# Kernel optimization log

Measured on AMD Instinct MI355X. Metric: run time of the kernel, lower is better.

## Reference

```python
import jax, jax.numpy as jnp
import numpy as np

BETA = 0.25
COMMIT_W = 1.0


def setup_inputs() -> dict:
    key = jax.random.key(0)
    ks = jax.random.split(key, 6)
    B, N, DIM, CDIM, K = 8, 1024, 256, 64, 16384
    z = jax.random.normal(ks[0], (B, N, DIM), dtype=jnp.float32)
    Wq = jax.random.normal(ks[1], (CDIM, DIM), dtype=jnp.float32) * (DIM ** -0.5)
    bq = jax.random.normal(ks[2], (CDIM,), dtype=jnp.float32) * 0.01
    # torch init: uniform(-1/K, 1/K)
    emb = jax.random.uniform(ks[3], (K, CDIM), dtype=jnp.float32, minval=-1.0 / K, maxval=1.0 / K)
    Wp = jax.random.normal(ks[4], (DIM, CDIM), dtype=jnp.float32) * (CDIM ** -0.5)
    bp = jax.random.normal(ks[5], (DIM,), dtype=jnp.float32) * 0.01
    return {"z": z, "Wq": Wq, "bq": bq, "emb": emb, "Wp": Wp, "bp": bp}


def reference(z, Wq, bq, emb, Wp, bp):
    # quant projection: [B,N,dim] -> [B,N,cdim]
    zp = jnp.einsum('bnd,cd->bnc', z, Wq) + bq
    # squared euclidean distances to codebook: [B,N,K]
    d = (jnp.sum(zp * zp, axis=2, keepdims=True)
         + jnp.sum(emb * emb, axis=1)
         - 2.0 * jnp.einsum('bnc,kc->bnk', zp, emb))
    sample_idxs = jnp.argmin(d, axis=2)              # [B,N] int
    z_q = emb[sample_idxs]                            # [B,N,cdim]
    commit_loss = (jnp.mean((jax.lax.stop_gradient(z_q) - zp) ** 2)
                   + BETA * jnp.mean((z_q - jax.lax.stop_gradient(zp)) ** 2))
    commit_loss = COMMIT_W * commit_loss
    # straight-through estimator
    z_q = zp + jax.lax.stop_gradient(z_q - zp)
    # post-quant projection: [B,N,cdim] -> [B,N,dim]
    out = jnp.einsum('bnc,dc->bnd', z_q, Wp) + bp
    return out, sample_idxs, commit_loss
```

## Files before the change

### kernel.cpp

```cpp
#include <hip/hip_runtime.h>
#include <hip/hip_bf16.h>


#define VWIN 1.0e-5f
#define CMAX 16

typedef short short8v __attribute__((ext_vector_type(8)));
typedef float floatx16 __attribute__((ext_vector_type(16)));

__device__ __forceinline__ short f2bf(float x) {
    unsigned u = __builtin_bit_cast(unsigned, x);
    unsigned r = (u + 0x7fffu + ((u >> 16) & 1u)) >> 16;
    return (short)r;
}

__device__ __forceinline__ float np_pairwise64_sq(const float* __restrict__ p) {
    #pragma clang fp contract(off)
    float v[16];
#pragma unroll
    for (int j = 0; j < 16; ++j) {
        float x0 = p[j]      * p[j];
        float x1 = p[j + 32] * p[j + 32];
        float x2 = p[j + 16] * p[j + 16];
        float x3 = p[j + 48] * p[j + 48];
        float r0 = x0 + x1;
        float r1 = x2 + x3;
        v[j] = r0 + r1;
    }
    float s[8], t[4];
#pragma unroll
    for (int j = 0; j < 8; ++j) s[j] = v[j] + v[j + 8];
#pragma unroll
    for (int j = 0; j < 4; ++j) t[j] = s[j] + s[j + 4];
    return (t[0] + t[2]) + (t[1] + t[3]);
}

__global__ __launch_bounds__(512) void k_prep(const float* __restrict__ z,
                                              const float* __restrict__ Wq,
                                              const float* __restrict__ bq,
                                              const float* __restrict__ emb,
                                              float* __restrict__ zp32,
                                              float* __restrict__ A32,
                                              short8v* __restrict__ zpf,
                                              float* __restrict__ B32,
                                              short8v* __restrict__ ef,
                                              float* __restrict__ bfl,
                                              float4* __restrict__ embT4,
                                              int tokblocks, int K) {
    __shared__ float pool[64 * 129 + 32 * 128 + 32 * 65];
    const int tid = threadIdx.x;
    const int bx  = blockIdx.x;

    if (bx < tokblocks) {
        float* wq  = pool;
        float* zl  = pool + 64 * 129;
        float* zps = zl + 32 * 128;
        const int w    = tid >> 6;
        const int lane = tid & 63;
        const int tbase = bx * 32;

        float l[4][4];
#pragma unroll
        for (int i = 0; i < 4; ++i)
#pragma unroll
            for (int j = 0; j < 4; ++j) l[i][j] = 0.f;

        for (int h = 0; h < 2; ++h) {
            __syncthreads();
            for (int i = tid; i < 64 * 128; i += 512) {
                const int c = i >> 7, m = i & 127;
                wq[c * 129 + m] = Wq[(size_t)c * 256 + h * 128 + m];
            }
            for (int i = tid; i < 32 * 128; i += 512) {
                const int t = i >> 7, m = i & 127;
                zl[t * 128 + m] = z[(size_t)(tbase + t) * 256 + h * 128 + m];
            }
            __syncthreads();
            {
                #pragma clang fp contract(off)
                const float* wr  = wq + lane * 129;
                const float* zt0 = zl + (w * 4 + 0) * 128;
                const float* zt1 = zl + (w * 4 + 1) * 128;
                const float* zt2 = zl + (w * 4 + 2) * 128;
                const float* zt3 = zl + (w * 4 + 3) * 128;
                for (int m = 0; m < 128; m += 4) {
                    const float w0 = wr[m], w1 = wr[m + 1], w2 = wr[m + 2], w3 = wr[m + 3];
                    const float4 p0 = *(const float4*)(zt0 + m);
                    const float4 p1 = *(const float4*)(zt1 + m);
                    const float4 p2 = *(const float4*)(zt2 + m);
                    const float4 p3 = *(const float4*)(zt3 + m);
                    l[0][0] += p0.x * w0; l[0][1] += p0.y * w1; l[0][2] += p0.z * w2; l[0][3] += p0.w * w3;
                    l[1][0] += p1.x * w0; l[1][1] += p1.y * w1; l[1][2] += p1.z * w2; l[1][3] += p1.w * w3;
                    l[2][0] += p2.x * w0; l[2][1] += p2.y * w1; l[2][2] += p2.z * w2; l[2][3] += p2.w * w3;
                    l[3][0] += p3.x * w0; l[3][1] += p3.y * w1; l[3][2] += p3.z * w2; l[3][3] += p3.w * w3;
                }
            }
        }
        {
            #pragma clang fp contract(off)
            const float bqc = bq[lane];
#pragma unroll
            for (int tk = 0; tk < 4; ++tk) {
                const float acc = (l[tk][0] + l[tk][1]) + (l[tk][2] + l[tk][3]);
                const float zpv = acc + bqc;
                zp32[(size_t)(tbase + w * 4 + tk) * 64 + lane] = zpv;
                zps[(w * 4 + tk) * 65 + lane] = zpv;
            }
        }
        __syncthreads();
        if (tid < 32) A32[tbase + tid] = np_pairwise64_sq(zps + tid * 65);
        if (tid < 256) {
            const int fl = tid & 63;
            const int s  = tid >> 6;
            const int row = fl & 31;
            const int k0 = s * 16 + (fl >> 5) * 8;
            short8v hv;
            const float* p = zps + row * 65 + k0;
#pragma unroll
            for (int j = 0; j < 8; ++j) hv[j] = f2bf(p[j]);
            zpf[(size_t)(bx * 4 + s) * 64 + fl] = hv;
        }
    } else {
        const int half = tid >> 8;
        const int ltid = tid & 255;
        const int tile = (bx - tokblocks) * 2 + half;
        float* et = pool + half * (32 * 65);

        for (int i = ltid; i < 2048; i += 256)
            et[(i >> 6) * 65 + (i & 63)] = emb[(size_t)tile * 2048 + i];
        __syncthreads();
        if (ltid < 32) {
            const float b = np_pairwise64_sq(et + ltid * 65);
            B32[tile * 32 + ltid] = b;
            const unsigned hb = (unsigned)(unsigned short)f2bf(-0.5f * b);
            bfl[tile * 32 + ltid] = __builtin_bit_cast(float, hb << 16);
        }
        {
            const int fl = ltid & 63;
            const int s  = ltid >> 6;
            const int row = fl & 31;
            const int k0 = s * 16 + (fl >> 5) * 8;
            short8v hv;
            const float* p = et + row * 65 + k0;
#pragma unroll
            for (int j = 0; j < 8; ++j) hv[j] = f2bf(p[j]);
            ef[(size_t)(tile * 4 + s) * 64 + fl] = hv;
        }
#pragma unroll
        for (int p = 0; p < 2; ++p) {
            const int id = ltid + (p << 8);
            const int m4 = id >> 5;
            const int r  = id & 31;
            const float* q = et + r * 65 + m4 * 4;
            float4 v;
            v.x = q[0]; v.y = q[1]; v.z = q[2]; v.w = q[3];
            embT4[(size_t)m4 * K + tile * 32 + r] = v;
        }
    }
}

__global__ __launch_bounds__(256) void k_scan_max(const short8v* __restrict__ zpf,
                                                  const short8v* __restrict__ ef,
                                                  const float* __restrict__ bfl,
                                                  float* __restrict__ pmax32,
                                                  float* __restrict__ pslice_t,
                                                  int tokens, int K) {
    __shared__ short8v s_ef[2048];
    __shared__ float s_bfl[256];
    const int tid  = threadIdx.x;
    const int w    = tid >> 6;
    const int lane = tid & 63;
    const int half = lane >> 5;
    const int col  = lane & 31;
    const int ttb  = (blockIdx.x * 4 + w) * 4;
    const int etiles = K / 2048;
    const int ct0 = blockIdx.y * etiles;

    for (int i = tid; i < etiles * 256; i += 256) s_ef[i] = ef[(size_t)ct0 * 256 + i];
    for (int i = tid; i < etiles * 32;  i += 256) s_bfl[i] = bfl[ct0 * 32 + i];

    short8v zh[4][4];
#pragma unroll
    for (int q = 0; q < 4; ++q)
#pragma unroll
        for (int s = 0; s < 4; ++s) zh[q][s] = zpf[(size_t)((ttb + q) * 4 + s) * 64 + lane];

    __syncthreads();

    float macc[4] = {-3.0e38f, -3.0e38f, -3.0e38f, -3.0e38f};

    for (int it = 0; it < etiles; ++it) {
        short8v eh[4];
#pragma unroll
        for (int s = 0; s < 4; ++s) eh[s] = s_ef[it * 256 + s * 64 + lane];
        floatx16 binit;
#pragma unroll
        for (int r = 0; r < 16; ++r)
            binit[r] = s_bfl[it * 32 + (r & 3) + 8 * (r >> 2) + 4 * half];
#pragma unroll
        for (int q = 0; q < 4; ++q) {
            floatx16 acc = __builtin_amdgcn_mfma_f32_32x32x16_bf16(eh[0], zh[q][0], binit, 0, 0, 0);
#pragma unroll
            for (int s = 1; s < 4; ++s)
                acc = __builtin_amdgcn_mfma_f32_32x32x16_bf16(eh[s], zh[q][s], acc, 0, 0, 0);
            float t0 = fmaxf(acc[0], acc[1]),  t1 = fmaxf(acc[2], acc[3]);
            float t2 = fmaxf(acc[4], acc[5]),  t3 = fmaxf(acc[6], acc[7]);
            float t4 = fmaxf(acc[8], acc[9]),  t5 = fmaxf(acc[10], acc[11]);
            float t6 = fmaxf(acc[12], acc[13]), t7 = fmaxf(acc[14], acc[15]);
            t0 = fmaxf(t0, t1); t2 = fmaxf(t2, t3); t4 = fmaxf(t4, t5); t6 = fmaxf(t6, t7);
            float tm = fmaxf(fmaxf(t0, t2), fmaxf(t4, t6));
            tm = fmaxf(tm, __shfl_xor(tm, 32));
            macc[q] = fmaxf(macc[q], tm);
            if (half == 0) {
                const int tok = (ttb + q) * 32 + col;
                pmax32[(size_t)(ct0 + it) * tokens + tok] = tm;
            }
        }
    }

    if (half == 0) {
#pragma unroll
        for (int q = 0; q < 4; ++q) {
            const int tok = (ttb + q) * 32 + col;
            pslice_t[(size_t)tok * 64 + blockIdx.y] = macc[q];
        }
    }
}

__global__ __launch_bounds__(256) void k_refine_ct(const float4* __restrict__ embT4,
                                                   const float* __restrict__ emb,
                                                   const float* __restrict__ zp32,
                                                   const float* __restrict__ A32,
                                                   const float* __restrict__ B32,
                                                   const float* __restrict__ pslice_t,
                                                   const float* __restrict__ pmax32,
                                                   int tokens, int CT, int K,
                                                   int* __restrict__ idx,
                                                   float* __restrict__ out_idx,
                                                   double* __restrict__ ploss) {
    #pragma clang fp contract(off)
    __shared__ __align__(16) float zps[8 * 64];
    __shared__ int s_cand[8][CMAX];
    const int tid = threadIdx.x;
    const int tbase = blockIdx.x * 8;
    for (int i = tid; i < 512; i += 256) zps[i] = zp32[(size_t)tbase * 64 + i];
    __syncthreads();

    const int w   = tid >> 6;
    const int ln  = tid & 31;
    const int sub = (tid >> 5) & 1;
    const int g   = w * 2 + sub;
    const int t   = tbase + g;
    const int shift = sub * 32;

    const float sv0 = pslice_t[(size_t)t * 64 + ln];
    const float sv1 = pslice_t[(size_t)t * 64 + 32 + ln];
    float m = fmaxf(sv0, sv1);
#pragma unroll
    for (int off = 16; off; off >>= 1) m = fmaxf(m, __shfl_xor(m, off, 32));
    const float thv = m - VWIN;

    const unsigned q0 = (unsigned)(__ballot(sv0 >= thv) >> shift);
    const unsigned q1 = (unsigned)(__ballot(sv1 >= thv) >> shift);
    unsigned long long qs = (unsigned long long)q0 | ((unsigned long long)q1 << 32);

    int ncand = 0;
    while (qs) {
        const int s = __builtin_ctzll(qs);
        qs &= qs - 1;
        float pv = -3.0e38f;
        if (ln < 8) pv = pmax32[(size_t)(s * 8 + ln) * tokens + t];
        unsigned cm = (unsigned)(__ballot(pv >= thv) >> shift) & 0xffu;
        while (cm) {
            const int c = __builtin_ctz(cm);
            cm &= cm - 1;
            if (ncand < CMAX && ln == 0) s_cand[g][ncand] = s * 8 + c;
            ++ncand;
        }
    }

    const bool full = (ncand > CMAX);
    const int iters = full ? CT : ncand;

    const float A = A32[t];
    const float* zp = zps + g * 64;

    float best = 3.0e38f;
    int bj = 0x7fffffff;
    for (int i = 0; i < iters; ++i) {
        const int ct = full ? i : s_cand[g][i];
        const int j  = ct * 32 + ln;
        const float Bj = B32[j];
        float l0 = 0.f, l1 = 0.f, l2 = 0.f, l3 = 0.f;
#pragma unroll
        for (int m4 = 0; m4 < 16; ++m4) {
            const float4 ev = embT4[(size_t)m4 * K + j];
            const float4 zv = *(const float4*)(zp + m4 * 4);
            l0 += zv.x * ev.x;
            l1 += zv.y * ev.y;
            l2 += zv.z * ev.z;
            l3 += zv.w * ev.w;
        }
        const float M = (l0 + l1) + (l2 + l3);
        const float S = A + Bj;
        const float d = S - 2.f * M;
        if (d < best) { best = d; bj = j; }
    }

#pragma unroll
    for (int off = 16; off; off >>= 1) {
        const float od = __shfl_xor(best, off, 32);
        const int   oj = __shfl_xor(bj, off, 32);
        if (od < best || (od == best && oj < bj)) { best = od; bj = oj; }
    }
    if ((unsigned)bj >= (unsigned)K) bj = 0;

    const float e0 = emb[(size_t)bj * 64 + ln];
    const float e1 = emb[(size_t)bj * 64 + 32 + ln];
    const float df0 = e0 - zp[ln];
    const float df1 = e1 - zp[32 + ln];
    double ls = (double)df0 * (double)df0 + (double)df1 * (double)df1;
#pragma unroll
    for (int off = 16; off; off >>= 1) ls += __shfl_xor(ls, off, 32);

    if (ln == 0) {
        idx[t] = bj;
        out_idx[t] = (float)bj;
        ploss[t] = ls;
    }
}

__global__ __launch_bounds__(256) void k_out_v2(const float* __restrict__ emb,
                                                const float* __restrict__ zp32,
                                                const int* __restrict__ idx,
                                                const float* __restrict__ Wp,
                                                const float* __restrict__ bp,
                                                float* __restrict__ out,
                                                const double* __restrict__ ploss,
                                                float* __restrict__ out_loss,
                                                int tokens, int K,
                                                double denom, int do_loss) {
    __shared__ float zq[8 * 64];
    __shared__ double red[256];
    const int tid = threadIdx.x;
    const int tbase = blockIdx.x * 8;
    for (int i = tid; i < 512; i += 256) {
        const int tk = i >> 6, c = i & 63;
        const int t = tbase + tk;
        int k = idx[t];
        if ((unsigned)k >= (unsigned)K) k = 0;
        const float zpv = zp32[(size_t)t * 64 + c];
        zq[i] = zpv + (emb[(size_t)k * 64 + c] - zpv);
    }
    float4 wp[16];
#pragma unroll
    for (int i = 0; i < 16; ++i) wp[i] = *(const float4*)(Wp + (size_t)tid * 64 + i * 4);
    const float bpd = bp[tid];
    __syncthreads();
#pragma unroll
    for (int tk = 0; tk < 8; ++tk) {
        const float* zr = zq + tk * 64;
        float acc = 0.f;
#pragma unroll
        for (int i = 0; i < 16; ++i) {
            const float4 p = *(const float4*)(zr + i * 4);
            acc += p.x * wp[i].x + p.y * wp[i].y + p.z * wp[i].z + p.w * wp[i].w;
        }
        out[(size_t)(tbase + tk) * 256 + tid] = acc + bpd;
    }
    if (do_loss && blockIdx.x == 0) {
        double a = 0.0;
        for (int i = tid; i < tokens; i += 256) a += ploss[i];
        red[tid] = a;
        __syncthreads();
        for (int s = 128; s > 0; s >>= 1) {
            if (tid < s) red[tid] += red[tid + s];
            __syncthreads();
        }
        if (tid == 0) *out_loss = (float)(1.25 * red[0] / denom);
    }
}

__global__ __launch_bounds__(256) void k_loss_red(const double* __restrict__ ploss,
                                                  float* __restrict__ out_loss,
                                                  int tokens, double denom) {
    __shared__ double red[256];
    double a = 0.0;
    for (int i = threadIdx.x; i < tokens; i += 256) a += ploss[i];
    red[threadIdx.x] = a;
    __syncthreads();
    for (int s = 128; s > 0; s >>= 1) {
        if (threadIdx.x < s) red[threadIdx.x] += red[threadIdx.x + s];
        __syncthreads();
    }
    if (threadIdx.x == 0) *out_loss = (float)(1.25 * red[0] / denom);
}

__global__ __launch_bounds__(64) void k_zp_np(const float* __restrict__ z,
                                              const float* __restrict__ Wq,
                                              const float* __restrict__ bq,
                                              float* __restrict__ zp32,
                                              int DIN, int CD) {
    #pragma clang fp contract(off)
    extern __shared__ float zl[];
    const int t = blockIdx.x;
    const int tid = threadIdx.x;
    for (int i = tid; i < DIN; i += 64) zl[i] = z[(size_t)t * DIN + i];
    __syncthreads();
    const int main8 = DIN & ~7;
    for (int c = tid; c < CD; c += 64) {
        const float* wr = Wq + (size_t)c * DIN;
        float l0 = 0.f, l1 = 0.f, l2 = 0.f, l3 = 0.f;
        for (int m = 0; m < main8; m += 4) {
            l0 += zl[m]     * wr[m];
            l1 += zl[m + 1] * wr[m + 1];
            l2 += zl[m + 2] * wr[m + 2];
            l3 += zl[m + 3] * wr[m + 3];
        }
        float acc = (l0 + l1) + (l2 + l3);
        for (int i = main8; i < DIN; ++i) acc += zl[i] * wr[i];
        zp32[(size_t)t * CD + c] = acc + bq[c];
    }
}

__global__ __launch_bounds__(256) void k_rowsum2_np(const float* __restrict__ src,
                                                    float* __restrict__ dst,
                                                    int rows) {
    #pragma clang fp contract(off)
    const int r = blockIdx.x * 256 + threadIdx.x;
    if (r >= rows) return;
    dst[r] = np_pairwise64_sq(src + (size_t)r * 64);
}

__global__ __launch_bounds__(256) void k_rowsum2_gen(const float* __restrict__ src,
                                                     float* __restrict__ dst,
                                                     int rows, int CD) {
    #pragma clang fp contract(off)
    const int r = blockIdx.x * 256 + threadIdx.x;
    if (r >= rows) return;
    const float* p = src + (size_t)r * CD;
    if (CD < 8) {
        float a = 0.f;
        for (int i = 0; i < CD; ++i) a += p[i] * p[i];
        dst[r] = a;
        return;
    }
    float acc[8];
#pragma unroll
    for (int j = 0; j < 8; ++j) acc[j] = p[j] * p[j];
    const int main8 = CD & ~7;
    for (int i = 8; i < main8; i += 8)
#pragma unroll
        for (int j = 0; j < 8; ++j) acc[j] += p[i + j] * p[i + j];
    float res = ((acc[0] + acc[1]) + (acc[2] + acc[3])) + ((acc[4] + acc[5]) + (acc[6] + acc[7]));
    for (int i = main8; i < CD; ++i) res += p[i] * p[i];
    dst[r] = res;
}

__global__ __launch_bounds__(256) void k_scan_gen(const float* __restrict__ emb,
                                                  const float* __restrict__ zp32,
                                                  const float* __restrict__ A32,
                                                  const float* __restrict__ B32,
                                                  int* __restrict__ idx,
                                                  float* __restrict__ out_idx,
                                                  int K, int CD) {
    #pragma clang fp contract(off)
    extern __shared__ float sm[];
    float* zp = sm;
    float* rm = zp + CD;
    int*   rj = (int*)(rm + 256);
    const int t = blockIdx.x;
    const int tid = threadIdx.x;
    for (int i = tid; i < CD; i += 256) zp[i] = zp32[(size_t)t * CD + i];
    __syncthreads();
    const float A = A32[t];
    float m1 = 3.0e38f; int j1 = 0x7fffffff;
    const int main8 = CD & ~7;
    for (int k = tid; k < K; k += 256) {
        const float* e = emb + (size_t)k * CD;
        float l0 = 0.f, l1 = 0.f, l2 = 0.f, l3 = 0.f;
        for (int m = 0; m < main8; m += 4) {
            l0 += zp[m]     * e[m];
            l1 += zp[m + 1] * e[m + 1];
            l2 += zp[m + 2] * e[m + 2];
            l3 += zp[m + 3] * e[m + 3];
        }
        float M = (l0 + l1) + (l2 + l3);
        for (int i = main8; i < CD; ++i) M += zp[i] * e[i];
        float S = A + B32[k];
        float d = S - 2.f * M;
        if (d < m1) { m1 = d; j1 = k; }
    }
    rm[tid] = m1; rj[tid] = j1;
    __syncthreads();
    if (tid == 0) {
        float gm = 3.0e38f; int gj = 0x7fffffff;
        for (int s = 0; s < 256; ++s) {
            if (rm[s] < gm || (rm[s] == gm && rj[s] < gj)) { gm = rm[s]; gj = rj[s]; }
        }
        idx[t] = gj;
        out_idx[t] = (float)gj;
    }
}

__global__ __launch_bounds__(256) void k_out(const float* __restrict__ emb,
                                             const float* __restrict__ zp32,
                                             const int* __restrict__ idx,
                                             const float* __restrict__ Wp,
                                             const float* __restrict__ bp,
                                             float* __restrict__ out,
                                             int DOUT, int CD) {
    extern __shared__ float zq[];
    const int t = blockIdx.x;
    const int tid = threadIdx.x;
    const int k = idx[t];
    for (int i = tid; i < CD; i += 256) {
        const float zpv = zp32[(size_t)t * CD + i];
        zq[i] = zpv + (emb[(size_t)k * CD + i] - zpv);
    }
    __syncthreads();
    for (int d = tid; d < DOUT; d += 256) {
        const float* w = Wp + (size_t)d * CD;
        float acc = 0.f;
        for (int c = 0; c < CD; ++c) acc += zq[c] * w[c];
        out[(size_t)t * DOUT + d] = acc + bp[d];
    }
}

__global__ __launch_bounds__(256) void k_loss1(const float* __restrict__ zp32,
                                               const float* __restrict__ emb,
                                               const int* __restrict__ idx,
                                               double* __restrict__ part,
                                               long long total, int CD) {
    double acc = 0.0;
    const long long stride = (long long)gridDim.x * 256;
    for (long long e = (long long)blockIdx.x * 256 + threadIdx.x; e < total; e += stride) {
        const long long t = e / CD;
        const int c = (int)(e - t * CD);
        const float df = emb[(size_t)idx[t] * CD + c] - zp32[e];
        acc += (double)df * (double)df;
    }
    __shared__ double red[256];
    red[threadIdx.x] = acc;
    __syncthreads();
    for (int s = 128; s > 0; s >>= 1) {
        if (threadIdx.x < s) red[threadIdx.x] += red[threadIdx.x + s];
        __syncthreads();
    }
    if (threadIdx.x == 0) part[blockIdx.x] = red[0];
}

__global__ __launch_bounds__(256) void k_loss2(const double* __restrict__ part,
                                               float* __restrict__ out_loss,
                                               double denom, int n) {
    __shared__ double red[256];
    const int tid = threadIdx.x;
    red[tid] = (tid < n) ? part[tid] : 0.0;
    __syncthreads();
    for (int s = 128; s > 0; s >>= 1) {
        if (tid < s) red[tid] += red[tid + s];
        __syncthreads();
    }
    if (tid == 0) *out_loss = (float)(1.25 * red[0] / denom);
}

extern "C" void kernel_launch(void* const* d_in, const int* in_sizes, int n_in,
                              void* d_out, int out_size, void* d_ws, size_t ws_size,
                              hipStream_t stream) {
    const float* z   = (const float*)d_in[0];
    const float* Wq  = (const float*)d_in[1];
    const float* bq  = (const float*)d_in[2];
    const float* emb = (const float*)d_in[3];
    const float* Wp  = (const float*)d_in[4];
    const float* bp  = (const float*)d_in[5];

    const int CD   = in_sizes[2];
    const int DIN  = in_sizes[1] / CD;
    const int DOUT = in_sizes[5];
    const int K    = in_sizes[3] / CD;
    const long long T = (long long)in_sizes[0] / DIN;

    float* out      = (float*)d_out;
    float* out_idx  = out + (size_t)T * DOUT;
    float* out_loss = out_idx + T;

    char* ws = (char*)d_ws;
    size_t off = 0;
    auto carve = [&](size_t bytes) -> char* {
        char* p = ws + off;
        off = (off + bytes + 255) & ~(size_t)255;
        return p;
    };
    float*  zp32  = (float*)carve((size_t)T * CD * 4);
    float*  A32   = (float*)carve((size_t)T * 4);
    float*  B32   = (float*)carve((size_t)K * 4);
    int*    idx   = (int*)carve((size_t)T * 4);
    double* part  = (double*)carve(128 * 8);
    double* ploss = (double*)carve((size_t)T * 8);

    bool fast = (CD == 64) && (DIN == 256) && (K % 2048 == 0) && (K <= 16384) &&
                (T % 512 == 0);
    short8v* zpf = nullptr; short8v* ef = nullptr;
    float* bfl = nullptr; float* pmax32 = nullptr; float* pslice_t = nullptr;
    float4* embT4 = nullptr;
    const int NSLICE = 64;
    const int CT = K / 32;
    if (fast) {
        const int ztiles = (int)(T / 32);
        const int ctiles = CT;
        zpf      = (short8v*)carve((size_t)ztiles * 256 * 16);
        ef       = (short8v*)carve((size_t)ctiles * 256 * 16);
        bfl      = (float*)carve((size_t)ctiles * 32 * 4);
        pmax32   = (float*)carve((size_t)CT * T * 4);
        pslice_t = (float*)carve((size_t)T * NSLICE * 4);
        embT4    = (float4*)carve((size_t)K * 64 * 4);
        if (off > ws_size) fast = false;
    }

    if (fast) {
        const int tokblocks  = (int)(T / 32);
        const int codeblocks = K / 64;
        k_prep<<<dim3((unsigned)(tokblocks + codeblocks)), dim3(512), 0, stream>>>(
            z, Wq, bq, emb, zp32, A32, zpf, B32, ef, bfl, embT4, tokblocks, K);

        dim3 grid((unsigned)(T / 512), NSLICE);
        k_scan_max<<<grid, dim3(256), 0, stream>>>(zpf, ef, bfl, pmax32, pslice_t,
                                                   (int)T, K);

        k_refine_ct<<<dim3((unsigned)(T / 8)), dim3(256), 0, stream>>>(
            embT4, emb, zp32, A32, B32, pslice_t, pmax32, (int)T, CT, K,
            idx, out_idx, ploss);

        if (DOUT == 256 && T % 8 == 0) {
            k_out_v2<<<dim3((unsigned)(T / 8)), dim3(256), 0, stream>>>(
                emb, zp32, idx, Wp, bp, out, ploss, out_loss, (int)T, K,
                (double)T * CD, 1);
        } else {
            k_loss_red<<<dim3(1), dim3(256), 0, stream>>>(ploss, out_loss, (int)T,
                                                          (double)T * CD);
            k_out<<<dim3((unsigned)T), dim3(256), (size_t)CD * 4, stream>>>(
                emb, zp32, idx, Wp, bp, out, DOUT, CD);
        }
    } else {
        k_zp_np<<<dim3((unsigned)T), dim3(64), (size_t)DIN * 4, stream>>>(z, Wq, bq, zp32, DIN, CD);
        if (CD == 64)
            k_rowsum2_np<<<dim3((unsigned)((T + 255) / 256)), dim3(256), 0, stream>>>(zp32, A32, (int)T);
        else
            k_rowsum2_gen<<<dim3((unsigned)((T + 255) / 256)), dim3(256), 0, stream>>>(zp32, A32, (int)T, CD);
        if (CD == 64)
            k_rowsum2_np<<<dim3((K + 255) / 256), dim3(256), 0, stream>>>(emb, B32, K);
        else
            k_rowsum2_gen<<<dim3((K + 255) / 256), dim3(256), 0, stream>>>(emb, B32, K, CD);

        const size_t sm = (size_t)CD * 4 + 256 * 4 + 256 * 4;
        k_scan_gen<<<dim3((unsigned)T), dim3(256), sm, stream>>>(
            emb, zp32, A32, B32, idx, out_idx, K, CD);
        k_loss1<<<dim3(128), dim3(256), 0, stream>>>(zp32, emb, idx, part, (long long)T * CD, CD);
        k_loss2<<<dim3(1), dim3(256), 0, stream>>>(part, out_loss, (double)T * CD, 128);

        if (DOUT == 256 && CD == 64 && T % 8 == 0) {
            k_out_v2<<<dim3((unsigned)(T / 8)), dim3(256), 0, stream>>>(
                emb, zp32, idx, Wp, bp, out, ploss, out_loss, (int)T, K,
                (double)T * CD, 0);
        } else {
            k_out<<<dim3((unsigned)T), dim3(256), (size_t)CD * 4, stream>>>(
                emb, zp32, idx, Wp, bp, out, DOUT, CD);
        }
    }
}
```

Measured before the change: 145.6 us.

## Fuse refine and output projection into one tail kernel with atomic loss reduction

Merges the candidate-refine kernel and the output projection kernel into a single k_tail launch. Indices and zp stay in shared memory instead of round-tripping through global buffers. The commit loss is now reduced with double atomics plus a last-block counter instead of a single-block serial pass over the per-token partials. It also stages global-to-LDS copies with global_load_lds and vectorizes the bias init and max-reduction in the scan kernel, adding dependence on atomic ordering and builtin availability.

```diff
diff --git a/kernel.cpp b/kernel.cpp
--- a/kernel.cpp
+++ b/kernel.cpp
@@ -7,6 +7,36 @@
 
 typedef short short8v __attribute__((ext_vector_type(8)));
 typedef float floatx16 __attribute__((ext_vector_type(16)));
+
+#ifndef __has_builtin
+#define __has_builtin(x) 0
+#endif
+#if __has_builtin(__builtin_amdgcn_global_load_lds)
+#define HAVE_GLL 1
+#else
+#define HAVE_GLL 0
+#endif
+
+__device__ __forceinline__ void stage16(const void* g, void* l, int lane) {
+#if HAVE_GLL
+    (void)lane;
+    __builtin_amdgcn_global_load_lds(
+        (const __attribute__((address_space(1))) void*)g,
+        (__attribute__((address_space(3))) void*)l, 16, 0, 0);
+#else
+    ((float4*)l)[lane] = *(const float4*)g;
+#endif
+}
+__device__ __forceinline__ void stage4(const void* g, void* l, int lane) {
+#if HAVE_GLL
+    (void)lane;
+    __builtin_amdgcn_global_load_lds(
+        (const __attribute__((address_space(1))) void*)g,
+        (__attribute__((address_space(3))) void*)l, 4, 0, 0);
+#else
+    ((float*)l)[lane] = *(const float*)g;
+#endif
+}
 
 __device__ __forceinline__ short f2bf(float x) {
     unsigned u = __builtin_bit_cast(unsigned, x);
@@ -46,10 +76,17 @@
                                               short8v* __restrict__ ef,
                                               float* __restrict__ bfl,
                                               float4* __restrict__ embT4,
+                                              double* __restrict__ loss_acc,
+                                              unsigned* __restrict__ loss_cnt,
                                               int tokblocks, int K) {
     __shared__ float pool[64 * 129 + 32 * 128 + 32 * 65];
     const int tid = threadIdx.x;
     const int bx  = blockIdx.x;
+
+    if (bx == 0) {
+        if (tid < 32) loss_acc[tid] = 0.0;
+        if (tid == 0) *loss_cnt = 0u;
+    }
 
     if (bx < tokblocks) {
         float* wq  = pool;
@@ -71,9 +108,11 @@
                 const int c = i >> 7, m = i & 127;
                 wq[c * 129 + m] = Wq[(size_t)c * 256 + h * 128 + m];
             }
-            for (int i = tid; i < 32 * 128; i += 512) {
-                const int t = i >> 7, m = i & 127;
-                zl[t * 128 + m] = z[(size_t)(tbase + t) * 256 + h * 128 + m];
+            for (int b4 = w * 64; b4 < 1024; b4 += 512) {
+                const int i4 = b4 + lane;
+                const int t  = i4 >> 5, m4 = i4 & 31;
+                stage16(z + (size_t)(tbase + t) * 256 + h * 128 + m4 * 4,
+                        zl + (size_t)b4 * 4, lane);
             }
             __syncthreads();
             {
@@ -165,8 +204,8 @@
                                                   float* __restrict__ pmax32,
                                                   float* __restrict__ pslice_t,
                                                   int tokens, int K) {
-    __shared__ short8v s_ef[2048];
-    __shared__ float s_bfl[256];
+    __shared__ __align__(16) short8v s_ef[2048];
+    __shared__ __align__(16) float s_bfl[256];
     const int tid  = threadIdx.x;
     const int w    = tid >> 6;
     const int lane = tid & 63;
@@ -176,8 +215,13 @@
     const int etiles = K / 2048;
     const int ct0 = blockIdx.y * etiles;
 
-    for (int i = tid; i < etiles * 256; i += 256) s_ef[i] = ef[(size_t)ct0 * 256 + i];
-    for (int i = tid; i < etiles * 32;  i += 256) s_bfl[i] = bfl[ct0 * 32 + i];
+    for (int base = w * 64; base < etiles * 256; base += 256)
+        stage16(&ef[(size_t)ct0 * 256 + base + lane], &s_ef[base], lane);
+    {
+        const int base = w * 64;
+        if (base + lane < etiles * 32)
+            stage4(&bfl[(size_t)ct0 * 32 + base + lane], &s_bfl[base], lane);
+    }
 
     short8v zh[4][4];
 #pragma unroll
@@ -193,22 +237,29 @@
         short8v eh[4];
 #pragma unroll
         for (int s = 0; s < 4; ++s) eh[s] = s_ef[it * 256 + s * 64 + lane];
+        const float4 b0 = *(const float4*)(s_bfl + it * 32 +  0 + 4 * half);
+        const float4 b1 = *(const float4*)(s_bfl + it * 32 +  8 + 4 * half);
+        const float4 b2 = *(const float4*)(s_bfl + it * 32 + 16 + 4 * half);
+        const float4 b3 = *(const float4*)(s_bfl + it * 32 + 24 + 4 * half);
         floatx16 binit;
-#pragma unroll
-        for (int r = 0; r < 16; ++r)
-            binit[r] = s_bfl[it * 32 + (r & 3) + 8 * (r >> 2) + 4 * half];
+        binit[0]  = b0.x; binit[1]  = b0.y; binit[2]  = b0.z; binit[3]  = b0.w;
+        binit[4]  = b1.x; binit[5]  = b1.y; binit[6]  = b1.z; binit[7]  = b1.w;
+        binit[8]  = b2.x; binit[9]  = b2.y; binit[10] = b2.z; binit[11] = b2.w;
+        binit[12] = b3.x; binit[13] = b3.y; binit[14] = b3.z; binit[15] = b3.w;
 #pragma unroll
         for (int q = 0; q < 4; ++q) {
             floatx16 acc = __builtin_amdgcn_mfma_f32_32x32x16_bf16(eh[0], zh[q][0], binit, 0, 0, 0);
 #pragma unroll
             for (int s = 1; s < 4; ++s)
                 acc = __builtin_amdgcn_mfma_f32_32x32x16_bf16(eh[s], zh[q][s], acc, 0, 0, 0);
-            float t0 = fmaxf(acc[0], acc[1]),  t1 = fmaxf(acc[2], acc[3]);
-            float t2 = fmaxf(acc[4], acc[5]),  t3 = fmaxf(acc[6], acc[7]);
-            float t4 = fmaxf(acc[8], acc[9]),  t5 = fmaxf(acc[10], acc[11]);
-            float t6 = fmaxf(acc[12], acc[13]), t7 = fmaxf(acc[14], acc[15]);
-            t0 = fmaxf(t0, t1); t2 = fmaxf(t2, t3); t4 = fmaxf(t4, t5); t6 = fmaxf(t6, t7);
-            float tm = fmaxf(fmaxf(t0, t2), fmaxf(t4, t6));
+            const float g0 = fmaxf(fmaxf(acc[0],  acc[1]),  acc[2]);
+            const float g1 = fmaxf(fmaxf(acc[3],  acc[4]),  acc[5]);
+            const float g2 = fmaxf(fmaxf(acc[6],  acc[7]),  acc[8]);
+            const float g3 = fmaxf(fmaxf(acc[9],  acc[10]), acc[11]);
+            const float g4 = fmaxf(fmaxf(acc[12], acc[13]), acc[14]);
+            const float h0 = fmaxf(fmaxf(g0, g1), g2);
+            const float h1 = fmaxf(fmaxf(g3, g4), acc[15]);
+            float tm = fmaxf(h0, h1);
             tm = fmaxf(tm, __shfl_xor(tm, 32));
             macc[q] = fmaxf(macc[q], tm);
             if (half == 0) {
@@ -227,130 +278,121 @@
     }
 }
 
-__global__ __launch_bounds__(256) void k_refine_ct(const float4* __restrict__ embT4,
-                                                   const float* __restrict__ emb,
-                                                   const float* __restrict__ zp32,
-                                                   const float* __restrict__ A32,
-                                                   const float* __restrict__ B32,
-                                                   const float* __restrict__ pslice_t,
-                                                   const float* __restrict__ pmax32,
-                                                   int tokens, int CT, int K,
-                                                   int* __restrict__ idx,
-                                                   float* __restrict__ out_idx,
-                                                   double* __restrict__ ploss) {
-    #pragma clang fp contract(off)
+__global__ __launch_bounds__(256) void k_tail(const float4* __restrict__ embT4,
+                                              const float* __restrict__ emb,
+                                              const float* __restrict__ zp32,
+                                              const float* __restrict__ A32,
+                                              const float* __restrict__ B32,
+                                              const float* __restrict__ pslice_t,
+                                              const float* __restrict__ pmax32,
+                                              const float* __restrict__ Wp,
+                                              const float* __restrict__ bp,
+                                              float* __restrict__ out,
+                                              float* __restrict__ out_idx,
+                                              int tokens, int CT, int K, double denom,
+                                              double* __restrict__ loss_acc,
+                                              unsigned* __restrict__ loss_cnt,
+                                              float* __restrict__ out_loss) {
     __shared__ __align__(16) float zps[8 * 64];
     __shared__ int s_cand[8][CMAX];
+    __shared__ int s_idx[8];
+    __shared__ double s_loss[8];
     const int tid = threadIdx.x;
     const int tbase = blockIdx.x * 8;
     for (int i = tid; i < 512; i += 256) zps[i] = zp32[(size_t)tbase * 64 + i];
     __syncthreads();
 
-    const int w   = tid >> 6;
-    const int ln  = tid & 31;
-    const int sub = (tid >> 5) & 1;
-    const int g   = w * 2 + sub;
-    const int t   = tbase + g;
-    const int shift = sub * 32;
-
-    const float sv0 = pslice_t[(size_t)t * 64 + ln];
-    const float sv1 = pslice_t[(size_t)t * 64 + 32 + ln];
-    float m = fmaxf(sv0, sv1);
-#pragma unroll
-    for (int off = 16; off; off >>= 1) m = fmaxf(m, __shfl_xor(m, off, 32));
-    const float thv = m - VWIN;
-
-    const unsigned q0 = (unsigned)(__ballot(sv0 >= thv) >> shift);
-    const unsigned q1 = (unsigned)(__ballot(sv1 >= thv) >> shift);
-    unsigned long long qs = (unsigned long long)q0 | ((unsigned long long)q1 << 32);
-
-    int ncand = 0;
-    while (qs) {
-        const int s = __builtin_ctzll(qs);
-        qs &= qs - 1;
-        float pv = -3.0e38f;
-        if (ln < 8) pv = pmax32[(size_t)(s * 8 + ln) * tokens + t];
-        unsigned cm = (unsigned)(__ballot(pv >= thv) >> shift) & 0xffu;
-        while (cm) {
-            const int c = __builtin_ctz(cm);
-            cm &= cm - 1;
-            if (ncand < CMAX && ln == 0) s_cand[g][ncand] = s * 8 + c;
-            ++ncand;
-        }
-    }
-
-    const bool full = (ncand > CMAX);
-    const int iters = full ? CT : ncand;
-
-    const float A = A32[t];
-    const float* zp = zps + g * 64;
-
-    float best = 3.0e38f;
-    int bj = 0x7fffffff;
-    for (int i = 0; i < iters; ++i) {
-        const int ct = full ? i : s_cand[g][i];
-        const int j  = ct * 32 + ln;
-        const float Bj = B32[j];
-        float l0 = 0.f, l1 = 0.f, l2 = 0.f, l3 = 0.f;
-#pragma unroll
-        for (int m4 = 0; m4 < 16; ++m4) {
-            const float4 ev = embT4[(size_t)m4 * K + j];
-            const float4 zv = *(const float4*)(zp + m4 * 4);
-            l0 += zv.x * ev.x;
-            l1 += zv.y * ev.y;
-            l2 += zv.z * ev.z;
-            l3 += zv.w * ev.w;
-        }
-        const float M = (l0 + l1) + (l2 + l3);
-        const float S = A + Bj;
-        const float d = S - 2.f * M;
-        if (d < best) { best = d; bj = j; }
-    }
-
-#pragma unroll
-    for (int off = 16; off; off >>= 1) {
-        const float od = __shfl_xor(best, off, 32);
-        const int   oj = __shfl_xor(bj, off, 32);
-        if (od < best || (od == best && oj < bj)) { best = od; bj = oj; }
-    }
-    if ((unsigned)bj >= (unsigned)K) bj = 0;
-
-    const float e0 = emb[(size_t)bj * 64 + ln];
-    const float e1 = emb[(size_t)bj * 64 + 32 + ln];
-    const float df0 = e0 - zp[ln];
-    const float df1 = e1 - zp[32 + ln];
-    double ls = (double)df0 * (double)df0 + (double)df1 * (double)df1;
-#pragma unroll
-    for (int off = 16; off; off >>= 1) ls += __shfl_xor(ls, off, 32);
-
-    if (ln == 0) {
-        idx[t] = bj;
-        out_idx[t] = (float)bj;
-        ploss[t] = ls;
-    }
-}
-
-__global__ __launch_bounds__(256) void k_out_v2(const float* __restrict__ emb,
-                                                const float* __restrict__ zp32,
-                                                const int* __restrict__ idx,
-                                                const float* __restrict__ Wp,
-                                                const float* __restrict__ bp,
-                                                float* __restrict__ out,
-                                                const double* __restrict__ ploss,
-                                                float* __restrict__ out_loss,
-                                                int tokens, int K,
-                                                double denom, int do_loss) {
-    __shared__ float zq[8 * 64];
-    __shared__ double red[256];
-    const int tid = threadIdx.x;
-    const int tbase = blockIdx.x * 8;
+    {
+        #pragma clang fp contract(off)
+        const int w   = tid >> 6;
+        const int ln  = tid & 31;
+        const int sub = (tid >> 5) & 1;
+        const int g   = w * 2 + sub;
+        const int t   = tbase + g;
+        const int shift = sub * 32;
+
+        const float sv0 = pslice_t[(size_t)t * 64 + ln];
+        const float sv1 = pslice_t[(size_t)t * 64 + 32 + ln];
+        float m = fmaxf(sv0, sv1);
+#pragma unroll
+        for (int off = 16; off; off >>= 1) m = fmaxf(m, __shfl_xor(m, off, 32));
+        const float thv = m - VWIN;
+
+        const unsigned q0 = (unsigned)(__ballot(sv0 >= thv) >> shift);
+        const unsigned q1 = (unsigned)(__ballot(sv1 >= thv) >> shift);
+        unsigned long long qs = (unsigned long long)q0 | ((unsigned long long)q1 << 32);
+
+        int ncand = 0;
+        while (qs) {
+            const int s = __builtin_ctzll(qs);
+            qs &= qs - 1;
+            float pv = -3.0e38f;
+            if (ln < 8) pv = pmax32[(size_t)(s * 8 + ln) * tokens + t];
+            unsigned cm = (unsigned)(__ballot(pv >= thv) >> shift) & 0xffu;
+            while (cm) {
+                const int c = __builtin_ctz(cm);
+                cm &= cm - 1;
+                if (ncand < CMAX && ln == 0) s_cand[g][ncand] = s * 8 + c;
+                ++ncand;
+            }
+        }
+
+        const bool full = (ncand > CMAX);
+        const int iters = full ? CT : ncand;
+
+        const float A = A32[t];
+        const float* zp = zps + g * 64;
+
+        float best = 3.0e38f;
+        int bj = 0x7fffffff;
+        for (int i = 0; i < iters; ++i) {
+            const int ct = full ? i : s_cand[g][i];
+            const int j  = ct * 32 + ln;
+            const float Bj = B32[j];
+            float l0 = 0.f, l1 = 0.f, l2 = 0.f, l3 = 0.f;
+#pragma unroll
+            for (int m4 = 0; m4 < 16; ++m4) {
+                const float4 ev = embT4[(size_t)m4 * K + j];
+                const float4 zv = *(const float4*)(zp + m4 * 4);
+                l0 += zv.x * ev.x;
+                l1 += zv.y * ev.y;
+                l2 += zv.z * ev.z;
+                l3 += zv.w * ev.w;
+            }
+            const float M = (l0 + l1) + (l2 + l3);
+            const float S = A + Bj;
+            const float d = S - 2.f * M;
+            if (d < best) { best = d; bj = j; }
+        }
+
+#pragma unroll
+        for (int off = 16; off; off >>= 1) {
+            const float od = __shfl_xor(best, off, 32);
+            const int   oj = __shfl_xor(bj, off, 32);
+            if (od < best || (od == best && oj < bj)) { best = od; bj = oj; }
+        }
+        if ((unsigned)bj >= (unsigned)K) bj = 0;
+
+        const float e0 = emb[(size_t)bj * 64 + ln];
+        const float e1 = emb[(size_t)bj * 64 + 32 + ln];
+        const float df0 = e0 - zp[ln];
+        const float df1 = e1 - zp[32 + ln];
+        double ls = (double)df0 * (double)df0 + (double)df1 * (double)df1;
+#pragma unroll
+        for (int off = 16; off; off >>= 1) ls += __shfl_xor(ls, off, 32);
+
+        if (ln == 0) {
+            s_idx[g] = bj;
+            out_idx[t] = (float)bj;
+            s_loss[g] = ls;
+        }
+    }
+    __syncthreads();
+
     for (int i = tid; i < 512; i += 256) {
         const int tk = i >> 6, c = i & 63;
-        const int t = tbase + tk;
-        int k = idx[t];
-        if ((unsigned)k >= (unsigned)K) k = 0;
-        const float zpv = zp32[(size_t)t * 64 + c];
-        zq[i] = zpv + (emb[(size_t)k * 64 + c] - zpv);
+        const float zpv = zps[i];
+        zps[i] = zpv + (emb[(size_t)s_idx[tk] * 64 + c] - zpv);
     }
     float4 wp[16];
 #pragma unroll
@@ -359,7 +401,7 @@
     __syncthreads();
 #pragma unroll
     for (int tk = 0; tk < 8; ++tk) {
-        const float* zr = zq + tk * 64;
+        const float* zr = zps + tk * 64;
         float acc = 0.f;
 #pragma unroll
         for (int i = 0; i < 16; ++i) {
@@ -368,32 +410,22 @@
         }
         out[(size_t)(tbase + tk) * 256 + tid] = acc + bpd;
     }
-    if (do_loss && blockIdx.x == 0) {
-        double a = 0.0;
-        for (int i = tid; i < tokens; i += 256) a += ploss[i];
-        red[tid] = a;
-        __syncthreads();
-        for (int s = 128; s > 0; s >>= 1) {
-            if (tid < s) red[tid] += red[tid + s];
-            __syncthreads();
-        }
-        if (tid == 0) *out_loss = (float)(1.25 * red[0] / denom);
-    }
-}
-
-__global__ __launch_bounds__(256) void k_loss_red(const double* __restrict__ ploss,
-                                                  float* __restrict__ out_loss,
-                                                  int tokens, double denom) {
-    __shared__ double red[256];
-    double a = 0.0;
-    for (int i = threadIdx.x; i < tokens; i += 256) a += ploss[i];
-    red[threadIdx.x] = a;
-    __syncthreads();
-    for (int s = 128; s > 0; s >>= 1) {
-        if (threadIdx.x < s) red[threadIdx.x] += red[threadIdx.x + s];
-        __syncthreads();
-    }
-    if (threadIdx.x == 0) *out_loss = (float)(1.25 * red[0] / denom);
+
+    if (tid == 0) {
+        double bs = 0.0;
+#pragma unroll
+        for (int i = 0; i < 8; ++i) bs += s_loss[i];
+        atomicAdd(&loss_acc[blockIdx.x & 31], bs);
+        __threadfence();
+        const unsigned old = atomicAdd(loss_cnt, 1u);
+        if (old == (unsigned)(gridDim.x - 1)) {
+            __threadfence();
+            double tot = 0.0;
+#pragma unroll
+            for (int i = 0; i < 32; ++i) tot += atomicAdd(&loss_acc[i], 0.0);
+            *out_loss = (float)(1.25 * tot / denom);
+        }
+    }
 }
 
 __global__ __launch_bounds__(64) void k_zp_np(const float* __restrict__ z,
@@ -596,13 +628,12 @@
     float*  B32   = (float*)carve((size_t)K * 4);
     int*    idx   = (int*)carve((size_t)T * 4);
     double* part  = (double*)carve(128 * 8);
-    double* ploss = (double*)carve((size_t)T * 8);
-
-    bool fast = (CD == 64) && (DIN == 256) && (K % 2048 == 0) && (K <= 16384) &&
-                (T % 512 == 0);
+
+    bool fast = (CD == 64) && (DIN == 256) && (DOUT == 256) && (K % 2048 == 0) &&
+                (K <= 16384) && (T % 512 == 0);
     short8v* zpf = nullptr; short8v* ef = nullptr;
     float* bfl = nullptr; float* pmax32 = nullptr; float* pslice_t = nullptr;
-    float4* embT4 = nullptr;
+    float4* embT4 = nullptr; double* loss_acc = nullptr; unsigned* loss_cnt = nullptr;
     const int NSLICE = 64;
     const int CT = K / 32;
     if (fast) {
@@ -614,6 +645,8 @@
         pmax32   = (float*)carve((size_t)CT * T * 4);
         pslice_t = (float*)carve((size_t)T * NSLICE * 4);
         embT4    = (float4*)carve((size_t)K * 64 * 4);
+        loss_acc = (double*)carve(32 * 8);
+        loss_cnt = (unsigned*)carve(256);
         if (off > ws_size) fast = false;
     }
 
@@ -621,26 +654,16 @@
         const int tokblocks  = (int)(T / 32);
         const int codeblocks = K / 64;
         k_prep<<<dim3((unsigned)(tokblocks + codeblocks)), dim3(512), 0, stream>>>(
-            z, Wq, bq, emb, zp32, A32, zpf, B32, ef, bfl, embT4, tokblocks, K);
+            z, Wq, bq, emb, zp32, A32, zpf, B32, ef, bfl, embT4,
+            loss_acc, loss_cnt, tokblocks, K);
 
         dim3 grid((unsigned)(T / 512), NSLICE);
         k_scan_max<<<grid, dim3(256), 0, stream>>>(zpf, ef, bfl, pmax32, pslice_t,
                                                    (int)T, K);
 
-        k_refine_ct<<<dim3((unsigned)(T / 8)), dim3(256), 0, stream>>>(
-            embT4, emb, zp32, A32, B32, pslice_t, pmax32, (int)T, CT, K,
-            idx, out_idx, ploss);
-
-        if (DOUT == 256 && T % 8 == 0) {
-            k_out_v2<<<dim3((unsigned)(T / 8)), dim3(256), 0, stream>>>(
-                emb, zp32, idx, Wp, bp, out, ploss, out_loss, (int)T, K,
-                (double)T * CD, 1);
-        } else {
-            k_loss_red<<<dim3(1), dim3(256), 0, stream>>>(ploss, out_loss, (int)T,
-                                                          (double)T * CD);
-            k_out<<<dim3((unsigned)T), dim3(256), (size_t)CD * 4, stream>>>(
-                emb, zp32, idx, Wp, bp, out, DOUT, CD);
-        }
+        k_tail<<<dim3((unsigned)(T / 8)), dim3(256), 0, stream>>>(
+            embT4, emb, zp32, A32, B32, pslice_t, pmax32, Wp, bp, out, out_idx,
+            (int)T, CT, K, (double)T * CD, loss_acc, loss_cnt, out_loss);
     } else {
         k_zp_np<<<dim3((unsigned)T), dim3(64), (size_t)DIN * 4, stream>>>(z, Wq, bq, zp32, DIN, CD);
         if (CD == 64)
@@ -658,13 +681,7 @@
         k_loss1<<<dim3(128), dim3(256), 0, stream>>>(zp32, emb, idx, part, (long long)T * CD, CD);
         k_loss2<<<dim3(1), dim3(256), 0, stream>>>(part, out_loss, (double)T * CD, 128);
 
-        if (DOUT == 256 && CD == 64 && T % 8 == 0) {
-            k_out_v2<<<dim3((unsigned)(T / 8)), dim3(256), 0, stream>>>(
-                emb, zp32, idx, Wp, bp, out, ploss, out_loss, (int)T, K,
-                (double)T * CD, 0);
-        } else {
-            k_out<<<dim3((unsigned)T), dim3(256), (size_t)CD * 4, stream>>>(
-                emb, zp32, idx, Wp, bp, out, DOUT, CD);
-        }
-    }
-}
+        k_out<<<dim3((unsigned)T), dim3(256), (size_t)CD * 4, stream>>>(
+            emb, zp32, idx, Wp, bp, out, DOUT, CD);
+    }
+}
```

After: 168.4 us. 15.7% more time.
